# Optimization experiments

Hardware: AMD Instinct MI355X
Metric: run time of the kernel (lower is better)

The kernel has to match this reference:

```python
import jax, jax.numpy as jnp
import numpy as np

LOG_VAR_Q = 0.0
TEMPERATURE = 0.5


def setup_inputs() -> dict:
    key = jax.random.key(0)
    k1, k2, k3 = jax.random.split(key, 3)
    bs, dim_z, W, H, K = 64, 64, 32, 32, 1024
    x = jax.random.normal(k1, (bs, dim_z, W, H), dtype=jnp.float32)
    codebook = jax.random.normal(k2, (K, dim_z), dtype=jnp.float32)
    log_var_q_scalar = jnp.asarray(0.0, dtype=jnp.float32)
    # pre-sampled standard Gumbel noise for the relaxed categorical
    u = jax.random.uniform(k3, (bs * W * H, K), dtype=jnp.float32,
                           minval=1e-6, maxval=1.0 - 1e-6)
    gumbel_noise = -jnp.log(-jnp.log(u))
    return {"x": x, "codebook": codebook,
            "log_var_q_scalar": log_var_q_scalar,
            "gumbel_noise": gumbel_noise}


def reference(x, codebook, log_var_q_scalar, gumbel_noise):
    bs, dim_z, W, H = x.shape
    # [bs, dim_z, W, H] -> [bs*W*H, dim_z]
    x_flat = jnp.transpose(x, (0, 2, 3, 1)).reshape(-1, dim_z)

    var_q = jnp.exp(jnp.asarray(LOG_VAR_Q, x.dtype)) + jnp.exp(log_var_q_scalar)
    precision_q = 1.0 / jnp.clip(var_q, 1e-10)
    w = 0.5 * precision_q  # scalar weight on squared distances

    sq_x = jnp.sum(x_flat * x_flat, axis=-1, keepdims=True)
    sq_c = jnp.sum(codebook * codebook, axis=-1)
    cross = jnp.einsum('nd,kd->nk', x_flat, codebook)
    logit = -w * (sq_x - 2.0 * cross + sq_c)

    log_probs = jax.nn.log_softmax(logit, axis=-1)
    probs = jnp.exp(log_probs)

    # gumbel-softmax relaxed one-hot encodings
    encodings = jax.nn.softmax((logit + gumbel_noise) / TEMPERATURE, axis=-1)

    quantized = jnp.einsum('nk,kd->nd', encodings, codebook)
    quantized = jnp.transpose(quantized.reshape(bs, W, H, dim_z), (0, 3, 1, 2))

    kld_discrete = jnp.sum(probs * log_probs) / bs
    kld_continuous = jnp.mean(jnp.sum(w * (x - quantized) ** 2, axis=(1, 2, 3)))
    return quantized, kld_discrete + kld_continuous
```

## Files before the change

### kernel.cpp

```cpp
#include <hip/hip_runtime.h>
#include <math.h>

#define K_CB 1024
#define D_Z  64
#define MT   32
#define NTOT 65536
#define NBLK (NTOT / MT)

typedef __attribute__((ext_vector_type(8)))  short s16x8;
typedef __attribute__((ext_vector_type(4)))  short s16x4;
typedef __attribute__((ext_vector_type(4)))  float f32x4;
typedef __attribute__((ext_vector_type(16))) float f32x16;

#define WS_CB16  0
#define WS_CBT16 131072
#define WS_NWSQC 262144
#define WS_PART  266240

__device__ __forceinline__ unsigned short f2b(float f) {
  unsigned int u = __float_as_uint(f);
  u += 0x7fffu + ((u >> 16) & 1u);
  return (unsigned short)(u >> 16);
}

__global__ void vq_prep(const float* __restrict__ cb, const float* __restrict__ lvq,
                        unsigned char* __restrict__ wsb) {
  unsigned short* cb16  = (unsigned short*)(wsb + WS_CB16);
  unsigned short* cbT16 = (unsigned short*)(wsb + WS_CBT16);
  float* nwsqc = (float*)(wsb + WS_NWSQC);
  const float w = 0.5f / fmaxf(1.0f + __expf(lvq[0]), 1e-10f);
  const int tid = threadIdx.x;
  const int k  = blockIdx.x * 16 + (tid >> 4);
  const int d0 = (tid & 15) * 4;
  const f32x4 v = *(const f32x4*)(cb + k * D_Z + d0);
  s16x4 b4;
  #pragma unroll
  for (int i = 0; i < 4; i++) b4[i] = (short)f2b(v[i]);
  *(s16x4*)(cb16 + k * D_Z + d0) = b4;
  #pragma unroll
  for (int i = 0; i < 4; i++) cbT16[(d0 + i) * K_CB + k] = (unsigned short)b4[i];
  float s = v[0]*v[0] + v[1]*v[1] + v[2]*v[2] + v[3]*v[3];
  #pragma unroll
  for (int off = 1; off < 16; off <<= 1) s += __shfl_xor(s, off);
  if ((tid & 15) == 0) nwsqc[k] = -w * s;
}

__global__ __launch_bounds__(512, 2)
void vq_main(const float* __restrict__ x, const float* __restrict__ gum,
             const float* __restrict__ lvq, unsigned char* __restrict__ wsb,
             float* __restrict__ out) {
  __shared__ __align__(16) unsigned short xa[MT * D_Z];
  __shared__ __align__(16) unsigned short es[MT * K_CB];
  __shared__ __align__(16) float stats[8][MT][4];
  __shared__ __align__(16) float s2s[8][MT];
  __shared__ float kldrow[MT];
  __shared__ float wred[8];

  const int tid  = threadIdx.x;
  const int w    = tid >> 6;
  const int lane = tid & 63;
  const int m32  = lane & 31;
  const int hi   = lane >> 5;
  const int bid  = blockIdx.x;
  const int blk  = ((bid & 7) << 8) | (bid >> 3);
  const int row0 = blk * MT;
  const int bidx = row0 >> 10;
  const int rem0 = row0 & 1023;
  const int kw0  = w << 7;

  const float wq = 0.5f / fmaxf(1.0f + __expf(lvq[0]), 1e-10f);
  const float w2 = 2.0f * wq;

  const unsigned short* cb16  = (const unsigned short*)(wsb + WS_CB16);
  const unsigned short* cbT16 = (const unsigned short*)(wsb + WS_CBT16);
  const float* nwsqc = (const float*)(wsb + WS_NWSQC);

  {
    const int m = tid & 31, dg = tid >> 5;
    #pragma unroll
    for (int i = 0; i < 4; i++) {
      const int d = dg + 16 * i;
      const float v = x[((bidx * D_Z + d) << 10) + rem0 + m];
      xa[(m * D_Z + d) ^ ((m & 7) << 3)] = f2b(v);
    }
  }
  __syncthreads();

  f32x16 acc[4];
  #pragma unroll
  for (int t = 0; t < 4; t++)
    #pragma unroll
    for (int r = 0; r < 16; r++) acc[t][r] = 0.f;

  const float* gp = gum + ((size_t)(row0 + m32) << 10) + kw0 + hi * 4;
  const unsigned short* ap = cb16 + (kw0 + m32) * D_Z + hi * 8;
  f32x4 gA[8], gB[8];
  s16x8 bx[4], af[8];

  #pragma unroll
  for (int kb = 0; kb < 4; kb++) {
    const int byteoff = (m32 * 128 + kb * 32 + hi * 16) ^ ((m32 & 7) << 4);
    bx[kb] = *(const s16x8*)((const unsigned char*)xa + byteoff);
  }
  #pragma unroll
  for (int i = 0; i < 8; i++) af[i] = *(const s16x8*)(ap + (i >> 2) * 2048 + (i & 3) * 16);
  #pragma unroll
  for (int u = 0; u < 8; u++) gA[u] = *(const f32x4*)(gp + (u >> 2) * 32 + (u & 3) * 8);
  #pragma unroll
  for (int i = 0; i < 8; i++)
    acc[i >> 2] = __builtin_amdgcn_mfma_f32_32x32x16_bf16(af[i], bx[i & 3], acc[i >> 2], 0, 0, 0);
  #pragma unroll
  for (int i = 0; i < 8; i++) af[i] = *(const s16x8*)(ap + (2 + (i >> 2)) * 2048 + (i & 3) * 16);
  #pragma unroll
  for (int u = 0; u < 8; u++) gB[u] = *(const f32x4*)(gp + 64 + (u >> 2) * 32 + (u & 3) * 8);
  #pragma unroll
  for (int i = 0; i < 8; i++)
    acc[2 + (i >> 2)] = __builtin_amdgcn_mfma_f32_32x32x16_bf16(af[i], bx[i & 3], acc[2 + (i >> 2)], 0, 0, 0);

  float m1 = -3.4e38f;
  #pragma unroll
  for (int t = 0; t < 4; t++) {
    #pragma unroll
    for (int q = 0; q < 4; q++) {
      const f32x4 nw = *(const f32x4*)(nwsqc + kw0 + t * 32 + q * 8 + hi * 4);
      #pragma unroll
      for (int i = 0; i < 4; i++) {
        acc[t][q * 4 + i] = fmaf(w2, acc[t][q * 4 + i], nw[i]);
        m1 = fmaxf(m1, acc[t][q * 4 + i]);
      }
    }
  }
  m1 = fmaxf(m1, __shfl_xor(m1, 32));

  float s1 = 0.f, Aa = 0.f;
  #pragma unroll
  for (int t = 0; t < 4; t++) {
    #pragma unroll
    for (int r = 0; r < 16; r++) {
      const float u = acc[t][r] - m1;
      const float e = __expf(u);
      s1 += e;
      Aa = fmaf(u, e, Aa);
    }
  }
  s1 += __shfl_xor(s1, 32);
  Aa += __shfl_xor(Aa, 32);

  float m2 = -3.4e38f;
  #pragma unroll
  for (int u = 0; u < 8; u++) {
    const int t = u >> 2, q = u & 3;
    #pragma unroll
    for (int i = 0; i < 4; i++) {
      const float z = 2.0f * (acc[t][q * 4 + i] + gA[u][i]);
      acc[t][q * 4 + i] = z;
      m2 = fmaxf(m2, z);
    }
  }
  #pragma unroll
  for (int u = 0; u < 8; u++) {
    const int t = 2 + (u >> 2), q = u & 3;
    #pragma unroll
    for (int i = 0; i < 4; i++) {
      const float z = 2.0f * (acc[t][q * 4 + i] + gB[u][i]);
      acc[t][q * 4 + i] = z;
      m2 = fmaxf(m2, z);
    }
  }
  m2 = fmaxf(m2, __shfl_xor(m2, 32));
  if (hi == 0) {
    f32x4 st = {m1, s1, Aa, m2};
    *(f32x4*)&stats[w][m32][0] = st;
  }
  __syncthreads();

  float M2 = -3.4e38f;
  {
    f32x4 st[8];
    #pragma unroll
    for (int q = 0; q < 8; q++) {
      st[q] = *(const f32x4*)&stats[q][m32][0];
      M2 = fmaxf(M2, st[q][3]);
    }
    if (w == 0) {
      float M1 = -3.4e38f;
      #pragma unroll
      for (int q = 0; q < 8; q++) M1 = fmaxf(M1, st[q][0]);
      float s1g = 0.f, Ag = 0.f;
      #pragma unroll
      for (int q = 0; q < 8; q++) {
        const float dm = st[q][0] - M1;
        const float c  = __expf(dm);
        s1g += c * st[q][1];
        Ag = fmaf(c, fmaf(dm, st[q][1], st[q][2]), Ag);
      }
      if (hi == 0) kldrow[m32] = Ag / s1g - __logf(s1g);
    }
  }

  float s2 = 0.f;
  #pragma unroll
  for (int t = 0; t < 4; t++) {
    #pragma unroll
    for (int q = 0; q < 4; q++) {
      float e[4];
      #pragma unroll
      for (int i = 0; i < 4; i++) {
        e[i] = __expf(acc[t][q * 4 + i] - M2);
        s2 += e[i];
      }
      const unsigned int p0 = (unsigned int)f2b(e[0]) | ((unsigned int)f2b(e[1]) << 16);
      const unsigned int p1 = (unsigned int)f2b(e[2]) | ((unsigned int)f2b(e[3]) << 16);
      const unsigned long long pk = (unsigned long long)p0 | ((unsigned long long)p1 << 32);
      const int byteoff = (m32 * 2048 + (kw0 + t * 32 + q * 8 + hi * 4) * 2) ^ ((m32 & 7) << 4);
      *(unsigned long long*)((unsigned char*)es + byteoff) = pk;
    }
  }
  s2 += __shfl_xor(s2, 32);
  if (hi == 0) s2s[w][m32] = s2;
  __syncthreads();

  const int m16 = lane & 15, g = lane >> 4;
  const int db = w >> 1, mb = w & 1;
  const int mrow = mb * 16 + m16;
  float s2g = 0.f;
  #pragma unroll
  for (int q = 0; q < 8; q++) s2g += s2s[q][mrow];
  const float inv2 = 1.0f / s2g;

  int offs[4];
  float xv[4];
  #pragma unroll
  for (int r = 0; r < 4; r++) {
    const int d = db * 16 + g * 4 + r;
    offs[r] = ((bidx * D_Z + d) << 10) + rem0 + mrow;
    xv[r] = x[offs[r]];
  }

  f32x4 qacc = (f32x4){0.f, 0.f, 0.f, 0.f};
  {
    const unsigned short* a2p = cbT16 + (db * 16 + m16) * K_CB + g * 8;
    const unsigned char* esb = (const unsigned char*)es;
    s16x8 a2b[2][4];
    #pragma unroll
    for (int j = 0; j < 4; j++) a2b[0][j] = *(const s16x8*)(a2p + j * 32);
    #pragma unroll
    for (int c = 0; c < 8; c++) {
      if (c < 7) {
        #pragma unroll
        for (int j = 0; j < 4; j++)
          a2b[(c + 1) & 1][j] = *(const s16x8*)(a2p + ((c + 1) * 4 + j) * 32);
      }
      #pragma unroll
      for (int j = 0; j < 4; j++) {
        const int kc = c * 4 + j;
        const int byteoff = (mrow * 2048 + kc * 64 + g * 16) ^ ((m16 & 7) << 4);
        const s16x8 b2 = *(const s16x8*)(esb + byteoff);
        qacc = __builtin_amdgcn_mfma_f32_16x16x32_bf16(a2b[c & 1][j], b2, qacc, 0, 0, 0);
      }
    }
  }

  float kca = 0.f;
  #pragma unroll
  for (int r = 0; r < 4; r++) {
    const float qv = qacc[r] * inv2;
    out[offs[r]] = qv;
    const float dx = xv[r] - qv;
    kca = fmaf(dx, dx, kca);
  }
  #pragma unroll
  for (int off = 1; off < 64; off <<= 1) kca += __shfl_xor(kca, off);
  if (lane == 0) wred[w] = kca;
  __syncthreads();
  if (tid == 0) {
    float tot = 0.f;
    #pragma unroll
    for (int q = 0; q < 8; q++) tot += wred[q];
    tot *= wq;
    #pragma unroll
    for (int i = 0; i < MT; i++) tot += kldrow[i];
    ((float*)(wsb + WS_PART))[blk] = tot;
  }
}

__global__ void vq_reduce(const unsigned char* __restrict__ wsb, float* __restrict__ out) {
  __shared__ float red[256];
  const float* part = (const float*)(wsb + WS_PART);
  const int t = threadIdx.x;
  float s = 0.f;
  for (int i = t; i < NBLK; i += 256) s += part[i];
  red[t] = s;
  __syncthreads();
  for (int st = 128; st > 0; st >>= 1) {
    if (t < st) red[t] += red[t + st];
    __syncthreads();
  }
  if (t == 0) out[NTOT * D_Z] = red[0] * (1.0f / 64.0f);
}

extern "C" void kernel_launch(void* const* d_in, const int* in_sizes, int n_in,
                              void* d_out, int out_size, void* d_ws, size_t ws_size,
                              hipStream_t stream) {
  const float* x   = (const float*)d_in[0];
  const float* cb  = (const float*)d_in[1];
  const float* lvq = (const float*)d_in[2];
  const float* gum = (const float*)d_in[3];
  float* out = (float*)d_out;
  unsigned char* wsb = (unsigned char*)d_ws;

  hipLaunchKernelGGL(vq_prep,   dim3(64),   dim3(256), 0, stream, cb, lvq, wsb);
  hipLaunchKernelGGL(vq_main,   dim3(NBLK), dim3(512), 0, stream, x, gum, lvq, wsb, out);
  hipLaunchKernelGGL(vq_reduce, dim3(1),    dim3(256), 0, stream, wsb, out);
}
```

Before: 186.5 us.

## Make main kernel persistent with register-resident codebook and prefetched Gumbel tiles

Converts vq_main into a persistent kernel of 512 blocks, each looping over four consecutive 32-row tiles. The codebook fragments and scaled norms now stay in registers across tiles, and the next tile's Gumbel noise is prefetched while the current tile finishes. The launch-bounds occupancy hint rises from 2 to 4. The intent is to amortise codebook loads and hide the Gumbel stream latency, but the extra register pressure from the resident codebook and doubled occupancy target risks spills, and the block-to-tile swizzle is dropped.

Result: slower. 520.3 us (+178.9%).

```diff
diff --git a/kernel.cpp b/kernel.cpp
--- a/kernel.cpp
+++ b/kernel.cpp
@@ -1,11 +1,13 @@
 #include <hip/hip_runtime.h>
 #include <math.h>
 
-#define K_CB 1024
-#define D_Z  64
-#define MT   32
-#define NTOT 65536
-#define NBLK (NTOT / MT)
+#define K_CB  1024
+#define D_Z   64
+#define MT    32
+#define NTOT  65536
+#define NTILE (NTOT / MT)
+#define NPERS 512
+#define TPB   (NTILE / NPERS)
 
 typedef __attribute__((ext_vector_type(8)))  short s16x8;
 typedef __attribute__((ext_vector_type(4)))  short s16x4;
@@ -45,7 +47,7 @@
   if ((tid & 15) == 0) nwsqc[k] = -w * s;
 }
 
-__global__ __launch_bounds__(512, 2)
+__global__ __launch_bounds__(512, 4)
 void vq_main(const float* __restrict__ x, const float* __restrict__ gum,
              const float* __restrict__ lvq, unsigned char* __restrict__ wsb,
              float* __restrict__ out) {
@@ -62,10 +64,6 @@
   const int m32  = lane & 31;
   const int hi   = lane >> 5;
   const int bid  = blockIdx.x;
-  const int blk  = ((bid & 7) << 8) | (bid >> 3);
-  const int row0 = blk * MT;
-  const int bidx = row0 >> 10;
-  const int rem0 = row0 & 1023;
   const int kw0  = w << 7;
 
   const float wq = 0.5f / fmaxf(1.0f + __expf(lvq[0]), 1e-10f);
@@ -75,212 +73,231 @@
   const unsigned short* cbT16 = (const unsigned short*)(wsb + WS_CBT16);
   const float* nwsqc = (const float*)(wsb + WS_NWSQC);
 
+  s16x8 cbf[16];
   {
-    const int m = tid & 31, dg = tid >> 5;
-    #pragma unroll
-    for (int i = 0; i < 4; i++) {
-      const int d = dg + 16 * i;
-      const float v = x[((bidx * D_Z + d) << 10) + rem0 + m];
-      xa[(m * D_Z + d) ^ ((m & 7) << 3)] = f2b(v);
-    }
+    const unsigned short* ap = cb16 + (kw0 + m32) * D_Z + hi * 8;
+    #pragma unroll
+    for (int t = 0; t < 4; t++)
+      #pragma unroll
+      for (int kb = 0; kb < 4; kb++)
+        cbf[t * 4 + kb] = *(const s16x8*)(ap + t * 2048 + kb * 16);
   }
-  __syncthreads();
-
-  f32x16 acc[4];
+  f32x4 nwf[16];
   #pragma unroll
   for (int t = 0; t < 4; t++)
     #pragma unroll
-    for (int r = 0; r < 16; r++) acc[t][r] = 0.f;
-
-  const float* gp = gum + ((size_t)(row0 + m32) << 10) + kw0 + hi * 4;
-  const unsigned short* ap = cb16 + (kw0 + m32) * D_Z + hi * 8;
-  f32x4 gA[8], gB[8];
-  s16x8 bx[4], af[8];
-
-  #pragma unroll
-  for (int kb = 0; kb < 4; kb++) {
-    const int byteoff = (m32 * 128 + kb * 32 + hi * 16) ^ ((m32 & 7) << 4);
-    bx[kb] = *(const s16x8*)((const unsigned char*)xa + byteoff);
+    for (int q = 0; q < 4; q++)
+      nwf[t * 4 + q] = *(const f32x4*)(nwsqc + kw0 + t * 32 + q * 8 + hi * 4);
+
+  f32x4 gg[16];
+  {
+    const float* gp = gum + ((size_t)(bid * TPB * MT + m32) << 10) + kw0 + hi * 4;
+    #pragma unroll
+    for (int u = 0; u < 16; u++)
+      gg[u] = *(const f32x4*)(gp + (u >> 2) * 32 + (u & 3) * 8);
   }
-  #pragma unroll
-  for (int i = 0; i < 8; i++) af[i] = *(const s16x8*)(ap + (i >> 2) * 2048 + (i & 3) * 16);
-  #pragma unroll
-  for (int u = 0; u < 8; u++) gA[u] = *(const f32x4*)(gp + (u >> 2) * 32 + (u & 3) * 8);
-  #pragma unroll
-  for (int i = 0; i < 8; i++)
-    acc[i >> 2] = __builtin_amdgcn_mfma_f32_32x32x16_bf16(af[i], bx[i & 3], acc[i >> 2], 0, 0, 0);
-  #pragma unroll
-  for (int i = 0; i < 8; i++) af[i] = *(const s16x8*)(ap + (2 + (i >> 2)) * 2048 + (i & 3) * 16);
-  #pragma unroll
-  for (int u = 0; u < 8; u++) gB[u] = *(const f32x4*)(gp + 64 + (u >> 2) * 32 + (u & 3) * 8);
-  #pragma unroll
-  for (int i = 0; i < 8; i++)
-    acc[2 + (i >> 2)] = __builtin_amdgcn_mfma_f32_32x32x16_bf16(af[i], bx[i & 3], acc[2 + (i >> 2)], 0, 0, 0);
-
-  float m1 = -3.4e38f;
-  #pragma unroll
-  for (int t = 0; t < 4; t++) {
-    #pragma unroll
-    for (int q = 0; q < 4; q++) {
-      const f32x4 nw = *(const f32x4*)(nwsqc + kw0 + t * 32 + q * 8 + hi * 4);
+  asm volatile("" ::: "memory");
+
+  #pragma unroll 1
+  for (int it = 0; it < TPB; ++it) {
+    const int tile = bid * TPB + it;
+    const int row0 = tile * MT;
+    const int bidx = row0 >> 10;
+    const int rem0 = row0 & 1023;
+
+    {
+      const int m = tid & 31, dg = tid >> 5;
       #pragma unroll
       for (int i = 0; i < 4; i++) {
-        acc[t][q * 4 + i] = fmaf(w2, acc[t][q * 4 + i], nw[i]);
-        m1 = fmaxf(m1, acc[t][q * 4 + i]);
-      }
-    }
-  }
-  m1 = fmaxf(m1, __shfl_xor(m1, 32));
-
-  float s1 = 0.f, Aa = 0.f;
-  #pragma unroll
-  for (int t = 0; t < 4; t++) {
-    #pragma unroll
-    for (int r = 0; r < 16; r++) {
-      const float u = acc[t][r] - m1;
-      const float e = __expf(u);
-      s1 += e;
-      Aa = fmaf(u, e, Aa);
-    }
-  }
-  s1 += __shfl_xor(s1, 32);
-  Aa += __shfl_xor(Aa, 32);
-
-  float m2 = -3.4e38f;
-  #pragma unroll
-  for (int u = 0; u < 8; u++) {
-    const int t = u >> 2, q = u & 3;
-    #pragma unroll
-    for (int i = 0; i < 4; i++) {
-      const float z = 2.0f * (acc[t][q * 4 + i] + gA[u][i]);
-      acc[t][q * 4 + i] = z;
-      m2 = fmaxf(m2, z);
-    }
-  }
-  #pragma unroll
-  for (int u = 0; u < 8; u++) {
-    const int t = 2 + (u >> 2), q = u & 3;
-    #pragma unroll
-    for (int i = 0; i < 4; i++) {
-      const float z = 2.0f * (acc[t][q * 4 + i] + gB[u][i]);
-      acc[t][q * 4 + i] = z;
-      m2 = fmaxf(m2, z);
-    }
-  }
-  m2 = fmaxf(m2, __shfl_xor(m2, 32));
-  if (hi == 0) {
-    f32x4 st = {m1, s1, Aa, m2};
-    *(f32x4*)&stats[w][m32][0] = st;
-  }
-  __syncthreads();
-
-  float M2 = -3.4e38f;
-  {
-    f32x4 st[8];
-    #pragma unroll
-    for (int q = 0; q < 8; q++) {
-      st[q] = *(const f32x4*)&stats[q][m32][0];
-      M2 = fmaxf(M2, st[q][3]);
-    }
-    if (w == 0) {
-      float M1 = -3.4e38f;
-      #pragma unroll
-      for (int q = 0; q < 8; q++) M1 = fmaxf(M1, st[q][0]);
-      float s1g = 0.f, Ag = 0.f;
+        const int d = dg + 16 * i;
+        const float v = x[((bidx * D_Z + d) << 10) + rem0 + m];
+        xa[(m * D_Z + d) ^ ((m & 7) << 3)] = f2b(v);
+      }
+    }
+    __syncthreads();
+
+    s16x8 bx[4];
+    #pragma unroll
+    for (int kb = 0; kb < 4; kb++) {
+      const int bo = (m32 * 128 + kb * 32 + hi * 16) ^ ((m32 & 7) << 4);
+      bx[kb] = *(const s16x8*)((const unsigned char*)xa + bo);
+    }
+    f32x16 acc[4];
+    #pragma unroll
+    for (int t = 0; t < 4; t++)
+      #pragma unroll
+      for (int r = 0; r < 16; r++) acc[t][r] = 0.f;
+    #pragma unroll
+    for (int t = 0; t < 4; t++)
+      #pragma unroll
+      for (int kb = 0; kb < 4; kb++)
+        acc[t] = __builtin_amdgcn_mfma_f32_32x32x16_bf16(cbf[t * 4 + kb], bx[kb], acc[t], 0, 0, 0);
+
+    float m1 = -3.4e38f;
+    #pragma unroll
+    for (int t = 0; t < 4; t++) {
+      #pragma unroll
+      for (int q = 0; q < 4; q++) {
+        #pragma unroll
+        for (int i = 0; i < 4; i++) {
+          acc[t][q * 4 + i] = fmaf(w2, acc[t][q * 4 + i], nwf[t * 4 + q][i]);
+          m1 = fmaxf(m1, acc[t][q * 4 + i]);
+        }
+      }
+    }
+    m1 = fmaxf(m1, __shfl_xor(m1, 32));
+
+    float s1 = 0.f, Aa = 0.f;
+    #pragma unroll
+    for (int t = 0; t < 4; t++) {
+      #pragma unroll
+      for (int r = 0; r < 16; r++) {
+        const float u = acc[t][r] - m1;
+        const float e = __expf(u);
+        s1 += e;
+        Aa = fmaf(u, e, Aa);
+      }
+    }
+    s1 += __shfl_xor(s1, 32);
+    Aa += __shfl_xor(Aa, 32);
+
+    float m2 = -3.4e38f;
+    #pragma unroll
+    for (int t = 0; t < 4; t++) {
+      #pragma unroll
+      for (int q = 0; q < 4; q++) {
+        #pragma unroll
+        for (int i = 0; i < 4; i++) {
+          const float z = 2.0f * (acc[t][q * 4 + i] + gg[t * 4 + q][i]);
+          acc[t][q * 4 + i] = z;
+          m2 = fmaxf(m2, z);
+        }
+      }
+    }
+
+    if (it + 1 < TPB) {
+      const float* gp = gum + ((size_t)(row0 + MT + m32) << 10) + kw0 + hi * 4;
+      #pragma unroll
+      for (int u = 0; u < 16; u++)
+        gg[u] = *(const f32x4*)(gp + (u >> 2) * 32 + (u & 3) * 8);
+    }
+    asm volatile("" ::: "memory");
+
+    m2 = fmaxf(m2, __shfl_xor(m2, 32));
+    if (hi == 0) {
+      f32x4 st = {m1, s1, Aa, m2};
+      *(f32x4*)&stats[w][m32][0] = st;
+    }
+    __syncthreads();
+
+    float M2 = -3.4e38f;
+    {
+      f32x4 st[8];
       #pragma unroll
       for (int q = 0; q < 8; q++) {
-        const float dm = st[q][0] - M1;
-        const float c  = __expf(dm);
-        s1g += c * st[q][1];
-        Ag = fmaf(c, fmaf(dm, st[q][1], st[q][2]), Ag);
-      }
-      if (hi == 0) kldrow[m32] = Ag / s1g - __logf(s1g);
-    }
-  }
-
-  float s2 = 0.f;
-  #pragma unroll
-  for (int t = 0; t < 4; t++) {
-    #pragma unroll
-    for (int q = 0; q < 4; q++) {
-      float e[4];
-      #pragma unroll
-      for (int i = 0; i < 4; i++) {
-        e[i] = __expf(acc[t][q * 4 + i] - M2);
-        s2 += e[i];
-      }
-      const unsigned int p0 = (unsigned int)f2b(e[0]) | ((unsigned int)f2b(e[1]) << 16);
-      const unsigned int p1 = (unsigned int)f2b(e[2]) | ((unsigned int)f2b(e[3]) << 16);
-      const unsigned long long pk = (unsigned long long)p0 | ((unsigned long long)p1 << 32);
-      const int byteoff = (m32 * 2048 + (kw0 + t * 32 + q * 8 + hi * 4) * 2) ^ ((m32 & 7) << 4);
-      *(unsigned long long*)((unsigned char*)es + byteoff) = pk;
-    }
-  }
-  s2 += __shfl_xor(s2, 32);
-  if (hi == 0) s2s[w][m32] = s2;
-  __syncthreads();
-
-  const int m16 = lane & 15, g = lane >> 4;
-  const int db = w >> 1, mb = w & 1;
-  const int mrow = mb * 16 + m16;
-  float s2g = 0.f;
-  #pragma unroll
-  for (int q = 0; q < 8; q++) s2g += s2s[q][mrow];
-  const float inv2 = 1.0f / s2g;
-
-  int offs[4];
-  float xv[4];
-  #pragma unroll
-  for (int r = 0; r < 4; r++) {
-    const int d = db * 16 + g * 4 + r;
-    offs[r] = ((bidx * D_Z + d) << 10) + rem0 + mrow;
-    xv[r] = x[offs[r]];
-  }
-
-  f32x4 qacc = (f32x4){0.f, 0.f, 0.f, 0.f};
-  {
-    const unsigned short* a2p = cbT16 + (db * 16 + m16) * K_CB + g * 8;
-    const unsigned char* esb = (const unsigned char*)es;
-    s16x8 a2b[2][4];
-    #pragma unroll
-    for (int j = 0; j < 4; j++) a2b[0][j] = *(const s16x8*)(a2p + j * 32);
-    #pragma unroll
-    for (int c = 0; c < 8; c++) {
-      if (c < 7) {
-        #pragma unroll
-        for (int j = 0; j < 4; j++)
-          a2b[(c + 1) & 1][j] = *(const s16x8*)(a2p + ((c + 1) * 4 + j) * 32);
-      }
-      #pragma unroll
-      for (int j = 0; j < 4; j++) {
-        const int kc = c * 4 + j;
-        const int byteoff = (mrow * 2048 + kc * 64 + g * 16) ^ ((m16 & 7) << 4);
-        const s16x8 b2 = *(const s16x8*)(esb + byteoff);
-        qacc = __builtin_amdgcn_mfma_f32_16x16x32_bf16(a2b[c & 1][j], b2, qacc, 0, 0, 0);
-      }
-    }
-  }
-
-  float kca = 0.f;
-  #pragma unroll
-  for (int r = 0; r < 4; r++) {
-    const float qv = qacc[r] * inv2;
-    out[offs[r]] = qv;
-    const float dx = xv[r] - qv;
-    kca = fmaf(dx, dx, kca);
-  }
-  #pragma unroll
-  for (int off = 1; off < 64; off <<= 1) kca += __shfl_xor(kca, off);
-  if (lane == 0) wred[w] = kca;
-  __syncthreads();
-  if (tid == 0) {
-    float tot = 0.f;
-    #pragma unroll
-    for (int q = 0; q < 8; q++) tot += wred[q];
-    tot *= wq;
-    #pragma unroll
-    for (int i = 0; i < MT; i++) tot += kldrow[i];
-    ((float*)(wsb + WS_PART))[blk] = tot;
+        st[q] = *(const f32x4*)&stats[q][m32][0];
+        M2 = fmaxf(M2, st[q][3]);
+      }
+      if (w == 0) {
+        float M1 = -3.4e38f;
+        #pragma unroll
+        for (int q = 0; q < 8; q++) M1 = fmaxf(M1, st[q][0]);
+        float s1g = 0.f, Ag = 0.f;
+        #pragma unroll
+        for (int q = 0; q < 8; q++) {
+          const float dm = st[q][0] - M1;
+          const float c  = __expf(dm);
+          s1g += c * st[q][1];
+          Ag = fmaf(c, fmaf(dm, st[q][1], st[q][2]), Ag);
+        }
+        if (hi == 0) kldrow[m32] = Ag / s1g - __logf(s1g);
+      }
+    }
+
+    float s2 = 0.f;
+    #pragma unroll
+    for (int t = 0; t < 4; t++) {
+      #pragma unroll
+      for (int q = 0; q < 4; q++) {
+        float e[4];
+        #pragma unroll
+        for (int i = 0; i < 4; i++) {
+          e[i] = __expf(acc[t][q * 4 + i] - M2);
+          s2 += e[i];
+        }
+        const unsigned int p0 = (unsigned int)f2b(e[0]) | ((unsigned int)f2b(e[1]) << 16);
+        const unsigned int p1 = (unsigned int)f2b(e[2]) | ((unsigned int)f2b(e[3]) << 16);
+        const unsigned long long pk = (unsigned long long)p0 | ((unsigned long long)p1 << 32);
+        const int byteoff = (m32 * 2048 + (kw0 + t * 32 + q * 8 + hi * 4) * 2) ^ ((m32 & 7) << 4);
+        *(unsigned long long*)((unsigned char*)es + byteoff) = pk;
+      }
+    }
+    s2 += __shfl_xor(s2, 32);
+    if (hi == 0) s2s[w][m32] = s2;
+    __syncthreads();
+
+    const int m16 = lane & 15, g = lane >> 4;
+    const int db = w >> 1, mb = w & 1;
+    const int mrow = mb * 16 + m16;
+    float s2g = 0.f;
+    #pragma unroll
+    for (int q = 0; q < 8; q++) s2g += s2s[q][mrow];
+    const float inv2 = 1.0f / s2g;
+
+    int offs[4];
+    float xv[4];
+    #pragma unroll
+    for (int r = 0; r < 4; r++) {
+      const int d = db * 16 + g * 4 + r;
+      offs[r] = ((bidx * D_Z + d) << 10) + rem0 + mrow;
+      xv[r] = x[offs[r]];
+    }
+
+    f32x4 qacc = (f32x4){0.f, 0.f, 0.f, 0.f};
+    {
+      const unsigned short* a2p = cbT16 + (db * 16 + m16) * K_CB + g * 8;
+      const unsigned char* esb = (const unsigned char*)es;
+      s16x8 a2b[2][4];
+      #pragma unroll
+      for (int j = 0; j < 4; j++) a2b[0][j] = *(const s16x8*)(a2p + j * 32);
+      #pragma unroll
+      for (int c = 0; c < 8; c++) {
+        if (c < 7) {
+          #pragma unroll
+          for (int j = 0; j < 4; j++)
+            a2b[(c + 1) & 1][j] = *(const s16x8*)(a2p + ((c + 1) * 4 + j) * 32);
+        }
+        #pragma unroll
+        for (int j = 0; j < 4; j++) {
+          const int kc = c * 4 + j;
+          const int byteoff = (mrow * 2048 + kc * 64 + g * 16) ^ ((m16 & 7) << 4);
+          const s16x8 b2 = *(const s16x8*)(esb + byteoff);
+          qacc = __builtin_amdgcn_mfma_f32_16x16x32_bf16(a2b[c & 1][j], b2, qacc, 0, 0, 0);
+        }
+      }
+    }
+
+    float kca = 0.f;
+    #pragma unroll
+    for (int r = 0; r < 4; r++) {
+      const float qv = qacc[r] * inv2;
+      out[offs[r]] = qv;
+      const float dx = xv[r] - qv;
+      kca = fmaf(dx, dx, kca);
+    }
+    #pragma unroll
+    for (int off = 1; off < 64; off <<= 1) kca += __shfl_xor(kca, off);
+    if (lane == 0) wred[w] = kca;
+    __syncthreads();
+    if (tid == 0) {
+      float tot = 0.f;
+      #pragma unroll
+      for (int q = 0; q < 8; q++) tot += wred[q];
+      tot *= wq;
+      #pragma unroll
+      for (int i = 0; i < MT; i++) tot += kldrow[i];
+      ((float*)(wsb + WS_PART))[tile] = tot;
+    }
   }
 }
 
@@ -289,7 +306,7 @@
   const float* part = (const float*)(wsb + WS_PART);
   const int t = threadIdx.x;
   float s = 0.f;
-  for (int i = t; i < NBLK; i += 256) s += part[i];
+  for (int i = t; i < NTILE; i += 256) s += part[i];
   red[t] = s;
   __syncthreads();
   for (int st = 128; st > 0; st >>= 1) {
@@ -309,7 +326,7 @@
   float* out = (float*)d_out;
   unsigned char* wsb = (unsigned char*)d_ws;
 
-  hipLaunchKernelGGL(vq_prep,   dim3(64),   dim3(256), 0, stream, cb, lvq, wsb);
-  hipLaunchKernelGGL(vq_main,   dim3(NBLK), dim3(512), 0, stream, x, gum, lvq, wsb, out);
-  hipLaunchKernelGGL(vq_reduce, dim3(1),    dim3(256), 0, stream, wsb, out);
-}
+  hipLaunchKernelGGL(vq_prep,   dim3(64),    dim3(256), 0, stream, cb, lvq, wsb);
+  hipLaunchKernelGGL(vq_main,   dim3(NPERS), dim3(512), 0, stream, x, gum, lvq, wsb, out);
+  hipLaunchKernelGGL(vq_reduce, dim3(1),     dim3(256), 0, stream, wsb, out);
+}
```
